# Performance work log

Measured on AMD Instinct MI355X. Metric: run time of the kernel, lower is better.

The kernel has to match this reference:

```python
import jax, jax.numpy as jnp
import numpy as np

B, C, N = 2, 6, 2048      # batch, channels (xyz+3 extra), points per cloud
K, NS = 64, 32            # top-k keypoints, ball-query group size
D = 32                    # deep feature dim (num_feat)
RADIUS = 1.0              # ball query radius (sample_and_group)
VR, VS = 1.0, 0.4         # voxelize range / step -> 6^3 = 216 candidates


def setup_inputs() -> dict:
    key = jax.random.key(0)
    ks = jax.random.split(key, 16)
    rn = lambda k, s, sc=1.0: jax.random.normal(k, s, dtype=jnp.float32) * sc
    Q, _ = jnp.linalg.qr(jax.random.normal(ks[2], (3, 3), dtype=jnp.float32))
    return {
        "src_pts": rn(ks[0], (B, C, N)),
        "tgt_pts": rn(ks[1], (B, C, N)),
        "R_init": Q,
        "t_init": rn(ks[3], (1, 3), 0.1),
        "W1": rn(ks[4], (C, 64), 0.2), "b1": jnp.zeros((64,), jnp.float32),
        "W2": rn(ks[5], (64, D), 0.2), "b2": jnp.zeros((D,), jnp.float32),
        "Wwl": rn(ks[6], (D, 1), 0.2), "bwl": jnp.zeros((1,), jnp.float32),
        "W3": rn(ks[7], (3 + D, 64), 0.2), "b3": jnp.zeros((64,), jnp.float32),
        "W4": rn(ks[8], (64, D), 0.2), "b4": jnp.zeros((D,), jnp.float32),
    }


def _fe(pts, W1, b1, W2, b2):
    # feat_extraction_layer: shared point-wise MLP. pts [B,C,N] -> xyz [B,N,3], feat [B,N,D]
    x = jnp.transpose(pts, (0, 2, 1))
    xyz = x[..., :3]
    f = jax.nn.relu(x @ W1 + b1)
    f = jax.nn.relu(f @ W2 + b2)
    return xyz, f


def _index_points(pts, idx):
    # pts [B,N,D], idx [B,K,S] -> [B,K,S,D]
    b = pts.shape[0]
    return pts[jnp.arange(b)[:, None, None], idx]


def _sqdist(a, b):
    # a [B,M,3], b [B,N,3] -> [B,M,N]
    return (jnp.sum(a * a, -1)[:, :, None] + jnp.sum(b * b, -1)[:, None, :]
            - 2.0 * jnp.einsum('bmd,bnd->bmn', a, b))


def reference(src_pts, tgt_pts, R_init, t_init, W1, b1, W2, b2, Wwl, bwl, W3, b3, W4, b4):
    b = src_pts.shape[0]
    # FE1 on source
    src_xyz, src_feat = _fe(src_pts, W1, b1, W2, b2)
    # weighting_layer: per-point saliency -> top-K keypoint indices
    w = (src_feat @ Wwl + bwl)[..., 0]                    # [B,N]
    _, kidx = jax.lax.top_k(w, K)                          # [B,K]
    src_T = jnp.transpose(src_pts, (0, 2, 1))              # [B,N,C]
    src_keypts = jnp.take_along_axis(src_T, kidx[:, :, None], axis=1)  # [B,K,C]
    centers = src_keypts[..., :3]
    # sample_and_group: ball query NS nearest-within-radius around each keypoint
    d2 = _sqdist(centers, src_xyz)                         # [B,K,N]
    negd, nn = jax.lax.top_k(-d2, NS)
    group_idx = jnp.where(-negd <= RADIUS ** 2, nn, nn[:, :, :1])
    grouped_xyz = _index_points(src_xyz, group_idx)        # [B,K,NS,3]
    keyfeats = _index_points(src_feat, group_idx)          # [B,K,NS,D]
    src_cat = jnp.concatenate([grouped_xyz - centers[:, :, None, :], keyfeats], -1)
    # FE1 on target
    tgt_xyz, tgt_feat = _fe(tgt_pts, W1, b1, W2, b2)
    # transform keypoints with initial pose, voxelize into candidate grid
    xform = jnp.einsum('ij,bkj->bki', R_init, centers) + t_init
    g = jnp.arange(int(2 * VR / VS) + 1, dtype=jnp.float32) * VS - VR   # 6 steps
    gx, gy, gz = jnp.meshgrid(g, g, g, indexing='ij')
    offs = jnp.stack([gx.ravel(), gy.ravel(), gz.ravel()], -1)          # [216,3]
    cand = xform[:, :, None, :] + offs                      # [B,K,216,3]
    nc = offs.shape[0]
    cand_flat = cand.reshape(b, K * nc, 3)
    # nearest target point per candidate -> gathered deep feature + relative offset
    d2t = _sqdist(cand_flat, tgt_xyz)                       # [B,K*216,N] (dominant buffer)
    nnt = jnp.argmin(d2t, axis=-1)                          # [B,K*216]
    nn_xyz = jnp.take_along_axis(tgt_xyz, nnt[:, :, None], axis=1)
    nn_feat = jnp.take_along_axis(tgt_feat, nnt[:, :, None], axis=1)
    rel = (nn_xyz - cand_flat).reshape(b, K, nc, 3)
    tgt_cat = jnp.concatenate([rel, nn_feat.reshape(b, K, nc, D)], -1)
    # DFE: shared MLP; src branch max-pools over the NS group
    dfe = lambda x: jax.nn.relu(jax.nn.relu(x @ W3 + b3) @ W4 + b4)
    src_dfe = jnp.max(dfe(src_cat), axis=2)                 # [B,K,D]
    tgt_dfe = dfe(tgt_cat)                                  # [B,K,216,D]
    # cpg: similarity -> softmax over candidates -> weighted centroid
    sim = jnp.einsum('bkd,bkcd->bkc', src_dfe, tgt_dfe)
    attn = jax.nn.softmax(sim, axis=-1)
    vcp = jnp.einsum('bkc,bkcd->bkd', attn, cand)           # [B,K,3]
    return src_keypts, vcp
```

## Files before the change

kernel.cpp:

```cpp
#include <hip/hip_runtime.h>
#include <math.h>

#define BB_ 2
#define CC_ 6
#define NN_ 2048
#define KK_ 64
#define NS_ 32
#define DD_ 32
#define NC_ 216
#define HH_ 64

#define OFF_SRC_PACK 0
#define OFF_TGT_PACK 16384
#define OFF_SRC_FEAT 32768
#define OFF_TGT_FEAT 163840
#define OFF_W        294912
#define OFF_CENTERS  299008
#define OFF_XFORM    299392
#define OFF_SRCDFE   299776
#define OFF_NNT      OFF_SRC_FEAT

__device__ __forceinline__ unsigned sortable_f32(float f) {
    unsigned u = __float_as_uint(f);
    return (u & 0x80000000u) ? ~u : (u | 0x80000000u);
}
__device__ __forceinline__ float unsortable_f32(unsigned s) {
    unsigned u = (s & 0x80000000u) ? (s ^ 0x80000000u) : ~s;
    return __uint_as_float(u);
}

__device__ __forceinline__ unsigned long long wave_sort64_asc(unsigned long long key, int lane) {
#pragma unroll
    for (int k = 2; k <= 64; k <<= 1) {
#pragma unroll
        for (int j = k >> 1; j > 0; j >>= 1) {
            unsigned long long other = __shfl_xor(key, j);
            bool lower = (lane & j) == 0;
            bool asc = (lane & k) == 0;
            bool takemin = (lower == asc);
            unsigned long long mn = key < other ? key : other;
            unsigned long long mx = key < other ? other : key;
            key = takemin ? mn : mx;
        }
    }
    return key;
}

__device__ __forceinline__ unsigned long long merge_keep_min64(unsigned long long a, unsigned long long b, int lane) {
    unsigned long long br = __shfl(b, 63 - lane);
    unsigned long long m = a < br ? a : br;
#pragma unroll
    for (int j = 32; j > 0; j >>= 1) {
        unsigned long long other = __shfl_xor(m, j);
        bool lower = (lane & j) == 0;
        unsigned long long mn = m < other ? m : other;
        unsigned long long mx = m < other ? other : m;
        m = lower ? mn : mx;
    }
    return m;
}

__device__ __forceinline__ void block_select64(unsigned long long kA, unsigned long long kB,
                                               unsigned long long* runs, int tid) {
    int w = tid >> 6, lane = tid & 63;
    kA = wave_sort64_asc(kA, lane);
    kB = wave_sort64_asc(kB, lane);
    unsigned long long m = merge_keep_min64(kA, kB, lane);
    runs[w * 64 + lane] = m;
    __syncthreads();
#pragma unroll
    for (int lvl = 8; lvl >= 1; lvl >>= 1) {
        unsigned long long r = 0;
        if (w < lvl) {
            unsigned long long a = runs[w * 64 + lane];
            unsigned long long b = runs[(w + lvl) * 64 + lane];
            r = merge_keep_min64(a, b, lane);
        }
        __syncthreads();
        if (w < lvl) runs[w * 64 + lane] = r;
        __syncthreads();
    }
}

__global__ void fe_kernel(const float* __restrict__ src, const float* __restrict__ tgt,
                          const float* __restrict__ W1, const float* __restrict__ b1,
                          const float* __restrict__ W2, const float* __restrict__ b2,
                          const float* __restrict__ Wwl, const float* __restrict__ bwl,
                          float* __restrict__ ws) {
    int tid = blockIdx.x * blockDim.x + threadIdx.x;
    if (tid >= 2 * BB_ * NN_) return;
    int cloud = tid / (BB_ * NN_);
    int r = tid - cloud * BB_ * NN_;
    int b = r / NN_, n = r % NN_;
    const float* pts = cloud ? tgt : src;
    float x[CC_];
#pragma unroll
    for (int c = 0; c < CC_; ++c) x[c] = pts[(b * CC_ + c) * NN_ + n];
    float bb;
    {
#pragma clang fp contract(off)
        bb = (x[0] * x[0] + x[1] * x[1]) + x[2] * x[2];
    }
    float4* pack = (float4*)(ws + (cloud ? OFF_TGT_PACK : OFF_SRC_PACK));
    pack[b * NN_ + n] = make_float4(x[0], x[1], x[2], bb);

    float h[HH_];
#pragma unroll
    for (int t = 0; t < HH_; ++t) {
        float s = b1[t];
#pragma unroll
        for (int c = 0; c < CC_; ++c) s += x[c] * W1[c * HH_ + t];
        h[t] = fmaxf(s, 0.f);
    }
    float* feat = ws + (cloud ? OFF_TGT_FEAT : OFF_SRC_FEAT) + (size_t)(b * NN_ + n) * DD_;
    float wsum = 0.f;
#pragma unroll 4
    for (int d = 0; d < DD_; ++d) {
        float s = b2[d];
#pragma unroll
        for (int t = 0; t < HH_; ++t) s += h[t] * W2[t * DD_ + d];
        s = fmaxf(s, 0.f);
        feat[d] = s;
        wsum += s * Wwl[d];
    }
    if (cloud == 0) (ws + OFF_W)[b * NN_ + n] = wsum + bwl[0];
}

__global__ void topk_kernel(const float* __restrict__ src, const float* __restrict__ R,
                            const float* __restrict__ t, float* __restrict__ ws,
                            float* __restrict__ out) {
    __shared__ unsigned long long runs[16 * 64];
    int b = blockIdx.x;
    int tid = threadIdx.x, w = tid >> 6, lane = tid & 63;
    const float* wv = ws + OFF_W + b * NN_;
    int jA = w * 128 + lane, jB = jA + 64;
    unsigned long long kA = ((unsigned long long)(~sortable_f32(wv[jA])) << 32) | (unsigned)jA;
    unsigned long long kB = ((unsigned long long)(~sortable_f32(wv[jB])) << 32) | (unsigned)jB;
    block_select64(kA, kB, runs, tid);
    if (tid < KK_) {
        int bi = (int)(runs[tid] & 0xFFFFFFFFu);
        float c3[3];
#pragma unroll
        for (int c = 0; c < CC_; ++c) {
            float v = src[(b * CC_ + c) * NN_ + bi];
            out[(b * KK_ + tid) * CC_ + c] = v;
            if (c < 3) c3[c] = v;
        }
        float* cen = ws + OFF_CENTERS + (b * KK_ + tid) * 3;
        cen[0] = c3[0]; cen[1] = c3[1]; cen[2] = c3[2];
        float* xf = ws + OFF_XFORM + (b * KK_ + tid) * 3;
#pragma unroll
        for (int i = 0; i < 3; ++i) {
#pragma clang fp contract(off)
            xf[i] = ((R[i * 3 + 0] * c3[0] + R[i * 3 + 1] * c3[1]) + R[i * 3 + 2] * c3[2]) + t[i];
        }
    }
}

__global__ void src_group_kernel(const float* __restrict__ W3, const float* __restrict__ b3,
                                 const float* __restrict__ W4, const float* __restrict__ b4,
                                 float* __restrict__ ws) {
    __shared__ unsigned long long runs[16 * 64];
    __shared__ float hs[NS_][HH_];
    __shared__ float outs[NS_][DD_];
    int bk = blockIdx.x;
    int b = bk / KK_;
    int tid = threadIdx.x, w = tid >> 6, lane = tid & 63;
    const float* cen = ws + OFF_CENTERS + bk * 3;
    float c0 = cen[0], c1 = cen[1], c2 = cen[2];
    float aa;
    {
#pragma clang fp contract(off)
        aa = (c0 * c0 + c1 * c1) + c2 * c2;
    }
    float m2x = -2.0f * c0, m2y = -2.0f * c1, m2z = -2.0f * c2;
    const float4* pack = (const float4*)(ws + OFF_SRC_PACK) + b * NN_;
    int jA = w * 128 + lane, jB = jA + 64;
    float4 pA = pack[jA], pB = pack[jB];
    float d2A, d2B;
    {
#pragma clang fp contract(off)
        d2A = (aa + pA.w) + ((m2x * pA.x + m2y * pA.y) + m2z * pA.z);
        d2B = (aa + pB.w) + ((m2x * pB.x + m2y * pB.y) + m2z * pB.z);
    }
    unsigned long long kA = ((unsigned long long)sortable_f32(d2A) << 32) | (unsigned)jA;
    unsigned long long kB = ((unsigned long long)sortable_f32(d2B) << 32) | (unsigned)jB;
    block_select64(kA, kB, runs, tid);
    const float* feats = ws + OFF_SRC_FEAT + (size_t)b * NN_ * DD_;
    unsigned long long key0 = runs[0];
#pragma unroll
    for (int ss = 0; ss < 2; ++ss) {
        int s = w * 2 + ss;
        unsigned long long key = runs[s];
        float dd = unsortable_f32((unsigned)(key >> 32));
        int j = (dd <= 1.0f) ? (int)(key & 0xFFFFFFFFu) : (int)(key0 & 0xFFFFFFFFu);
        float4 p = pack[j];
        float r0 = p.x - c0, r1 = p.y - c1, r2 = p.z - c2;
        const float* f = feats + (size_t)j * DD_;
        float acc = b3[lane] + r0 * W3[0 * HH_ + lane] + r1 * W3[1 * HH_ + lane] + r2 * W3[2 * HH_ + lane];
#pragma unroll 8
        for (int d = 0; d < DD_; ++d) acc += f[d] * W3[(3 + d) * HH_ + lane];
        hs[s][lane] = fmaxf(acc, 0.f);
    }
    __syncthreads();
    {
        int s2 = tid >> 5, di = tid & 31;
        float o = b4[di];
#pragma unroll 8
        for (int t2 = 0; t2 < HH_; ++t2) o += hs[s2][t2] * W4[t2 * DD_ + di];
        outs[s2][di] = fmaxf(o, 0.f);
    }
    __syncthreads();
    if (tid < DD_) {
        float m = -INFINITY;
#pragma unroll 8
        for (int s = 0; s < NS_; ++s) m = fmaxf(m, outs[s][tid]);
        (ws + OFF_SRCDFE)[bk * DD_ + tid] = m;
    }
}

__global__ void cand_nn_kernel(float* __restrict__ ws) {
    __shared__ float4 pk[NN_];
    int blk = blockIdx.x;
    int bk = blk >> 1;
    int half = blk & 1;
    int b = bk / KK_;
    int tid = threadIdx.x;
    const float4* pack = (const float4*)(ws + OFF_TGT_PACK) + b * NN_;
    for (int j = tid; j < NN_; j += 576) {
        pk[j ^ ((j >> 6) & 7)] = pack[j];
    }
    const float* xf = ws + OFF_XFORM + bk * 3;
    float x0 = xf[0], x1 = xf[1], x2 = xf[2];
    __syncthreads();

    int lg = tid >> 5;
    int chunk = tid & 31;
    int grp = half * 18 + lg;
    int ix = grp / 6, iy = grp % 6;
    float cx = x0 + (ix * 0.4f - 1.0f);
    float cy = x1 + (iy * 0.4f - 1.0f);
    float cxy2;
    {
#pragma clang fp contract(off)
        cxy2 = cx * cx + cy * cy;
    }
    float m2x = -2.0f * cx, m2y = -2.0f * cy;
    float aaz[6], m2z[6];
#pragma unroll
    for (int z = 0; z < 6; ++z) {
        float cz = x2 + (z * 0.4f - 1.0f);
        {
#pragma clang fp contract(off)
            aaz[z] = cxy2 + cz * cz;
        }
        m2z[z] = -2.0f * cz;
    }
    float bv[6];
    int bi[6];
#pragma unroll
    for (int z = 0; z < 6; ++z) { bv[z] = INFINITY; bi[z] = 0; }
    int base = chunk * 64;
    int sw = chunk & 7;
    for (int i = 0; i < 64; ++i) {
        int j = base + i;
        float4 p = pk[base + (i ^ sw)];
        float txy;
        {
#pragma clang fp contract(off)
            txy = m2x * p.x + m2y * p.y;
        }
#pragma unroll
        for (int z = 0; z < 6; ++z) {
            float d2;
            {
#pragma clang fp contract(off)
                d2 = (aaz[z] + p.w) + (txy + m2z[z] * p.z);
            }
            if (d2 < bv[z]) { bv[z] = d2; bi[z] = j; }
        }
    }
    int* nnt = (int*)ws + OFF_NNT + bk * NC_ + grp * 6;
#pragma unroll
    for (int z = 0; z < 6; ++z) {
        unsigned long long key = ((unsigned long long)sortable_f32(bv[z]) << 32) | (unsigned)bi[z];
#pragma unroll
        for (int m = 1; m <= 16; m <<= 1) {
            unsigned long long other = __shfl_xor(key, m);
            key = other < key ? other : key;
        }
        if (chunk == 0) nnt[z] = (int)(key & 0xFFFFFFFFu);
    }
}

__global__ void simvcp_kernel(const float* __restrict__ W3, const float* __restrict__ b3,
                              const float* __restrict__ W4, const float* __restrict__ b4,
                              float* __restrict__ ws, float* __restrict__ out) {
    __shared__ float sims[NC_];
    int bk = blockIdx.x;
    int b = bk / KK_;
    int tid = threadIdx.x;
    const float* xf = ws + OFF_XFORM + bk * 3;
    if (tid < NC_) {
        int c = tid;
        int ix = c / 36, iy = (c / 6) % 6, iz = c % 6;
        float cx = xf[0] + (ix * 0.4f - 1.0f);
        float cy = xf[1] + (iy * 0.4f - 1.0f);
        float cz = xf[2] + (iz * 0.4f - 1.0f);
        int bi = ((const int*)ws)[OFF_NNT + bk * NC_ + c];
        float4 p = ((const float4*)(ws + OFF_TGT_PACK))[b * NN_ + bi];
        float x[3 + DD_];
        x[0] = p.x - cx; x[1] = p.y - cy; x[2] = p.z - cz;
        const float* f = ws + OFF_TGT_FEAT + ((size_t)b * NN_ + bi) * DD_;
#pragma unroll
        for (int d = 0; d < DD_; ++d) x[3 + d] = f[d];
        float o[DD_];
#pragma unroll
        for (int d = 0; d < DD_; ++d) o[d] = b4[d];
        for (int t = 0; t < HH_; ++t) {
            float acc = b3[t];
#pragma unroll
            for (int cc = 0; cc < 3 + DD_; ++cc) acc += x[cc] * W3[cc * HH_ + t];
            float ht = fmaxf(acc, 0.f);
#pragma unroll
            for (int d = 0; d < DD_; ++d) o[d] += ht * W4[t * DD_ + d];
        }
        const float* sd = ws + OFF_SRCDFE + bk * DD_;
        float sim = 0.f;
#pragma unroll
        for (int d = 0; d < DD_; ++d) sim += fmaxf(o[d], 0.f) * sd[d];
        sims[c] = sim;
    }
    __syncthreads();
    if (tid < 64) {
        int lane = tid;
        float m = -INFINITY;
        for (int c = lane; c < NC_; c += 64) m = fmaxf(m, sims[c]);
#pragma unroll
        for (int sh = 32; sh; sh >>= 1) m = fmaxf(m, __shfl_xor(m, sh));
        float se = 0.f, v0 = 0.f, v1 = 0.f, v2 = 0.f;
        for (int c = lane; c < NC_; c += 64) {
            float e = expf(sims[c] - m);
            int ix = c / 36, iy = (c / 6) % 6, iz = c % 6;
            se += e;
            v0 += e * (xf[0] + (ix * 0.4f - 1.0f));
            v1 += e * (xf[1] + (iy * 0.4f - 1.0f));
            v2 += e * (xf[2] + (iz * 0.4f - 1.0f));
        }
#pragma unroll
        for (int sh = 32; sh; sh >>= 1) {
            se += __shfl_xor(se, sh);
            v0 += __shfl_xor(v0, sh);
            v1 += __shfl_xor(v1, sh);
            v2 += __shfl_xor(v2, sh);
        }
        if (lane == 0) {
            float inv = 1.0f / se;
            float* oo = out + BB_ * KK_ * CC_ + bk * 3;
            oo[0] = v0 * inv;
            oo[1] = v1 * inv;
            oo[2] = v2 * inv;
        }
    }
}

extern "C" void kernel_launch(void* const* d_in, const int* in_sizes, int n_in,
                              void* d_out, int out_size, void* d_ws, size_t ws_size,
                              hipStream_t stream) {
    const float* src = (const float*)d_in[0];
    const float* tgt = (const float*)d_in[1];
    const float* R   = (const float*)d_in[2];
    const float* t   = (const float*)d_in[3];
    const float* W1  = (const float*)d_in[4];
    const float* b1  = (const float*)d_in[5];
    const float* W2  = (const float*)d_in[6];
    const float* b2  = (const float*)d_in[7];
    const float* Wwl = (const float*)d_in[8];
    const float* bwl = (const float*)d_in[9];
    const float* W3  = (const float*)d_in[10];
    const float* b3  = (const float*)d_in[11];
    const float* W4  = (const float*)d_in[12];
    const float* b4  = (const float*)d_in[13];
    float* ws  = (float*)d_ws;
    float* out = (float*)d_out;

    fe_kernel<<<(2 * BB_ * NN_ + 127) / 128, 128, 0, stream>>>(src, tgt, W1, b1, W2, b2, Wwl, bwl, ws);
    topk_kernel<<<BB_, 1024, 0, stream>>>(src, R, t, ws, out);
    src_group_kernel<<<BB_ * KK_, 1024, 0, stream>>>(W3, b3, W4, b4, ws);
    cand_nn_kernel<<<BB_ * KK_ * 2, 576, 0, stream>>>(ws);
    simvcp_kernel<<<BB_ * KK_, 256, 0, stream>>>(W3, b3, W4, b4, ws, out);
}
```

Measured before the change: 88.92 us.

## Merge source grouping and candidate NN search into one heterogeneous kernel

Combines src_group_kernel and cand_nn_kernel into a single launch. The first 256 blocks do the candidate nearest-neighbour search and the remaining 128 blocks do ball-query grouping plus the DFE max-pool. The grouping path is reworked for 576 threads: 8 waves each sort four 64-key runs, and the merge tree is shallower. NNT output moves to its own workspace offset so it no longer aliases source features, which both branches now use concurrently. This removes one launch and lets the two independent stages overlap, at the cost of shared-memory union sizing and uneven block work.

```diff
diff --git a/kernel.cpp b/kernel.cpp
--- a/kernel.cpp
+++ b/kernel.cpp
@@ -18,7 +18,7 @@
 #define OFF_CENTERS  299008
 #define OFF_XFORM    299392
 #define OFF_SRCDFE   299776
-#define OFF_NNT      OFF_SRC_FEAT
+#define OFF_NNT      303872
 
 __device__ __forceinline__ unsigned sortable_f32(float f) {
     unsigned u = __float_as_uint(f);
@@ -60,8 +60,8 @@
     return m;
 }
 
-__device__ __forceinline__ void block_select64(unsigned long long kA, unsigned long long kB,
-                                               unsigned long long* runs, int tid) {
+__device__ __forceinline__ void block_select64_16w(unsigned long long kA, unsigned long long kB,
+                                                   unsigned long long* runs, int tid) {
     int w = tid >> 6, lane = tid & 63;
     kA = wave_sort64_asc(kA, lane);
     kB = wave_sort64_asc(kB, lane);
@@ -136,7 +136,7 @@
     int jA = w * 128 + lane, jB = jA + 64;
     unsigned long long kA = ((unsigned long long)(~sortable_f32(wv[jA])) << 32) | (unsigned)jA;
     unsigned long long kB = ((unsigned long long)(~sortable_f32(wv[jB])) << 32) | (unsigned)jB;
-    block_select64(kA, kB, runs, tid);
+    block_select64_16w(kA, kB, runs, tid);
     if (tid < KK_) {
         int bi = (int)(runs[tid] & 0xFFFFFFFFu);
         float c3[3];
@@ -157,139 +157,164 @@
     }
 }
 
-__global__ void src_group_kernel(const float* __restrict__ W3, const float* __restrict__ b3,
-                                 const float* __restrict__ W4, const float* __restrict__ b4,
-                                 float* __restrict__ ws) {
-    __shared__ unsigned long long runs[16 * 64];
-    __shared__ float hs[NS_][HH_];
-    __shared__ float outs[NS_][DD_];
-    int bk = blockIdx.x;
-    int b = bk / KK_;
-    int tid = threadIdx.x, w = tid >> 6, lane = tid & 63;
-    const float* cen = ws + OFF_CENTERS + bk * 3;
-    float c0 = cen[0], c1 = cen[1], c2 = cen[2];
-    float aa;
-    {
-#pragma clang fp contract(off)
-        aa = (c0 * c0 + c1 * c1) + c2 * c2;
-    }
-    float m2x = -2.0f * c0, m2y = -2.0f * c1, m2z = -2.0f * c2;
-    const float4* pack = (const float4*)(ws + OFF_SRC_PACK) + b * NN_;
-    int jA = w * 128 + lane, jB = jA + 64;
-    float4 pA = pack[jA], pB = pack[jB];
-    float d2A, d2B;
-    {
-#pragma clang fp contract(off)
-        d2A = (aa + pA.w) + ((m2x * pA.x + m2y * pA.y) + m2z * pA.z);
-        d2B = (aa + pB.w) + ((m2x * pB.x + m2y * pB.y) + m2z * pB.z);
-    }
-    unsigned long long kA = ((unsigned long long)sortable_f32(d2A) << 32) | (unsigned)jA;
-    unsigned long long kB = ((unsigned long long)sortable_f32(d2B) << 32) | (unsigned)jB;
-    block_select64(kA, kB, runs, tid);
-    const float* feats = ws + OFF_SRC_FEAT + (size_t)b * NN_ * DD_;
-    unsigned long long key0 = runs[0];
-#pragma unroll
-    for (int ss = 0; ss < 2; ++ss) {
-        int s = w * 2 + ss;
-        unsigned long long key = runs[s];
-        float dd = unsortable_f32((unsigned)(key >> 32));
-        int j = (dd <= 1.0f) ? (int)(key & 0xFFFFFFFFu) : (int)(key0 & 0xFFFFFFFFu);
-        float4 p = pack[j];
-        float r0 = p.x - c0, r1 = p.y - c1, r2 = p.z - c2;
-        const float* f = feats + (size_t)j * DD_;
-        float acc = b3[lane] + r0 * W3[0 * HH_ + lane] + r1 * W3[1 * HH_ + lane] + r2 * W3[2 * HH_ + lane];
+__global__ __launch_bounds__(576) void mid_kernel(const float* __restrict__ W3, const float* __restrict__ b3,
+                                                  const float* __restrict__ W4, const float* __restrict__ b4,
+                                                  float* __restrict__ ws) {
+    __shared__ union U {
+        float4 pk[NN_];
+        struct {
+            unsigned long long runs[8 * 64];
+            float hs[NS_][HH_];
+            float outs[NS_][DD_];
+        } s;
+    } u;
+    int blk = blockIdx.x;
+    int tid = threadIdx.x;
+    if (blk < 2 * BB_ * KK_) {
+        int bk = blk >> 1;
+        int half = blk & 1;
+        int b = bk / KK_;
+        const float4* pack = (const float4*)(ws + OFF_TGT_PACK) + b * NN_;
+        for (int j = tid; j < NN_; j += 576) {
+            u.pk[j ^ ((j >> 6) & 7)] = pack[j];
+        }
+        const float* xf = ws + OFF_XFORM + bk * 3;
+        float x0 = xf[0], x1 = xf[1], x2 = xf[2];
+        __syncthreads();
+
+        int lg = tid >> 5;
+        int chunk = tid & 31;
+        int grp = half * 18 + lg;
+        int ix = grp / 6, iy = grp % 6;
+        float cx = x0 + (ix * 0.4f - 1.0f);
+        float cy = x1 + (iy * 0.4f - 1.0f);
+        float cxy2;
+        {
+#pragma clang fp contract(off)
+            cxy2 = cx * cx + cy * cy;
+        }
+        float m2x = -2.0f * cx, m2y = -2.0f * cy;
+        float aaz[6], m2z[6];
+#pragma unroll
+        for (int z = 0; z < 6; ++z) {
+            float cz = x2 + (z * 0.4f - 1.0f);
+            {
+#pragma clang fp contract(off)
+                aaz[z] = cxy2 + cz * cz;
+            }
+            m2z[z] = -2.0f * cz;
+        }
+        float bv[6];
+        int bi[6];
+#pragma unroll
+        for (int z = 0; z < 6; ++z) { bv[z] = INFINITY; bi[z] = 0; }
+        int base = chunk * 64;
+        int sw = chunk & 7;
+        for (int i = 0; i < 64; ++i) {
+            int j = base + i;
+            float4 p = u.pk[base + (i ^ sw)];
+            float txy;
+            {
+#pragma clang fp contract(off)
+                txy = m2x * p.x + m2y * p.y;
+            }
+#pragma unroll
+            for (int z = 0; z < 6; ++z) {
+                float d2;
+                {
+#pragma clang fp contract(off)
+                    d2 = (aaz[z] + p.w) + (txy + m2z[z] * p.z);
+                }
+                if (d2 < bv[z]) { bv[z] = d2; bi[z] = j; }
+            }
+        }
+        int* nnt = (int*)ws + OFF_NNT + bk * NC_ + grp * 6;
+#pragma unroll
+        for (int z = 0; z < 6; ++z) {
+            unsigned long long key = ((unsigned long long)sortable_f32(bv[z]) << 32) | (unsigned)bi[z];
+#pragma unroll
+            for (int m = 1; m <= 16; m <<= 1) {
+                unsigned long long other = __shfl_xor(key, m);
+                key = other < key ? other : key;
+            }
+            if (chunk == 0) nnt[z] = (int)(key & 0xFFFFFFFFu);
+        }
+    } else {
+        int bk = blk - 2 * BB_ * KK_;
+        int b = bk / KK_;
+        int w = tid >> 6, lane = tid & 63;
+        const float* cen = ws + OFF_CENTERS + bk * 3;
+        float c0 = cen[0], c1 = cen[1], c2 = cen[2];
+        float aa;
+        {
+#pragma clang fp contract(off)
+            aa = (c0 * c0 + c1 * c1) + c2 * c2;
+        }
+        float m2x = -2.0f * c0, m2y = -2.0f * c1, m2z = -2.0f * c2;
+        const float4* pack = (const float4*)(ws + OFF_SRC_PACK) + b * NN_;
+        if (w < 8) {
+            unsigned long long k4[4];
+#pragma unroll
+            for (int q = 0; q < 4; ++q) {
+                int j = w * 256 + q * 64 + lane;
+                float4 p = pack[j];
+                float d2;
+                {
+#pragma clang fp contract(off)
+                    d2 = (aa + p.w) + ((m2x * p.x + m2y * p.y) + m2z * p.z);
+                }
+                k4[q] = ((unsigned long long)sortable_f32(d2) << 32) | (unsigned)j;
+            }
+            unsigned long long m1 = merge_keep_min64(wave_sort64_asc(k4[0], lane),
+                                                     wave_sort64_asc(k4[1], lane), lane);
+            unsigned long long m2 = merge_keep_min64(wave_sort64_asc(k4[2], lane),
+                                                     wave_sort64_asc(k4[3], lane), lane);
+            u.s.runs[w * 64 + lane] = merge_keep_min64(m1, m2, lane);
+        }
+        __syncthreads();
+#pragma unroll
+        for (int lvl = 4; lvl >= 1; lvl >>= 1) {
+            unsigned long long r = 0;
+            if (w < lvl) {
+                r = merge_keep_min64(u.s.runs[w * 64 + lane], u.s.runs[(w + lvl) * 64 + lane], lane);
+            }
+            __syncthreads();
+            if (w < lvl) u.s.runs[w * 64 + lane] = r;
+            __syncthreads();
+        }
+        const float* feats = ws + OFF_SRC_FEAT + (size_t)b * NN_ * DD_;
+        unsigned long long key0 = u.s.runs[0];
+        if (w < 8) {
+#pragma unroll
+            for (int ss = 0; ss < 4; ++ss) {
+                int s = w * 4 + ss;
+                unsigned long long key = u.s.runs[s];
+                float dd = unsortable_f32((unsigned)(key >> 32));
+                int j = (dd <= 1.0f) ? (int)(key & 0xFFFFFFFFu) : (int)(key0 & 0xFFFFFFFFu);
+                float4 p = pack[j];
+                float r0 = p.x - c0, r1 = p.y - c1, r2 = p.z - c2;
+                const float* f = feats + (size_t)j * DD_;
+                float acc = b3[lane] + r0 * W3[0 * HH_ + lane] + r1 * W3[1 * HH_ + lane] + r2 * W3[2 * HH_ + lane];
 #pragma unroll 8
-        for (int d = 0; d < DD_; ++d) acc += f[d] * W3[(3 + d) * HH_ + lane];
-        hs[s][lane] = fmaxf(acc, 0.f);
-    }
-    __syncthreads();
-    {
-        int s2 = tid >> 5, di = tid & 31;
-        float o = b4[di];
+                for (int d = 0; d < DD_; ++d) acc += f[d] * W3[(3 + d) * HH_ + lane];
+                u.s.hs[s][lane] = fmaxf(acc, 0.f);
+            }
+        }
+        __syncthreads();
+        for (int idx = tid; idx < NS_ * DD_; idx += 576) {
+            int s2 = idx >> 5, di = idx & 31;
+            float o = b4[di];
 #pragma unroll 8
-        for (int t2 = 0; t2 < HH_; ++t2) o += hs[s2][t2] * W4[t2 * DD_ + di];
-        outs[s2][di] = fmaxf(o, 0.f);
-    }
-    __syncthreads();
-    if (tid < DD_) {
-        float m = -INFINITY;
+            for (int t2 = 0; t2 < HH_; ++t2) o += u.s.hs[s2][t2] * W4[t2 * DD_ + di];
+            u.s.outs[s2][di] = fmaxf(o, 0.f);
+        }
+        __syncthreads();
+        if (tid < DD_) {
+            float m = -INFINITY;
 #pragma unroll 8
-        for (int s = 0; s < NS_; ++s) m = fmaxf(m, outs[s][tid]);
-        (ws + OFF_SRCDFE)[bk * DD_ + tid] = m;
-    }
-}
-
-__global__ void cand_nn_kernel(float* __restrict__ ws) {
-    __shared__ float4 pk[NN_];
-    int blk = blockIdx.x;
-    int bk = blk >> 1;
-    int half = blk & 1;
-    int b = bk / KK_;
-    int tid = threadIdx.x;
-    const float4* pack = (const float4*)(ws + OFF_TGT_PACK) + b * NN_;
-    for (int j = tid; j < NN_; j += 576) {
-        pk[j ^ ((j >> 6) & 7)] = pack[j];
-    }
-    const float* xf = ws + OFF_XFORM + bk * 3;
-    float x0 = xf[0], x1 = xf[1], x2 = xf[2];
-    __syncthreads();
-
-    int lg = tid >> 5;
-    int chunk = tid & 31;
-    int grp = half * 18 + lg;
-    int ix = grp / 6, iy = grp % 6;
-    float cx = x0 + (ix * 0.4f - 1.0f);
-    float cy = x1 + (iy * 0.4f - 1.0f);
-    float cxy2;
-    {
-#pragma clang fp contract(off)
-        cxy2 = cx * cx + cy * cy;
-    }
-    float m2x = -2.0f * cx, m2y = -2.0f * cy;
-    float aaz[6], m2z[6];
-#pragma unroll
-    for (int z = 0; z < 6; ++z) {
-        float cz = x2 + (z * 0.4f - 1.0f);
-        {
-#pragma clang fp contract(off)
-            aaz[z] = cxy2 + cz * cz;
-        }
-        m2z[z] = -2.0f * cz;
-    }
-    float bv[6];
-    int bi[6];
-#pragma unroll
-    for (int z = 0; z < 6; ++z) { bv[z] = INFINITY; bi[z] = 0; }
-    int base = chunk * 64;
-    int sw = chunk & 7;
-    for (int i = 0; i < 64; ++i) {
-        int j = base + i;
-        float4 p = pk[base + (i ^ sw)];
-        float txy;
-        {
-#pragma clang fp contract(off)
-            txy = m2x * p.x + m2y * p.y;
-        }
-#pragma unroll
-        for (int z = 0; z < 6; ++z) {
-            float d2;
-            {
-#pragma clang fp contract(off)
-                d2 = (aaz[z] + p.w) + (txy + m2z[z] * p.z);
-            }
-            if (d2 < bv[z]) { bv[z] = d2; bi[z] = j; }
-        }
-    }
-    int* nnt = (int*)ws + OFF_NNT + bk * NC_ + grp * 6;
-#pragma unroll
-    for (int z = 0; z < 6; ++z) {
-        unsigned long long key = ((unsigned long long)sortable_f32(bv[z]) << 32) | (unsigned)bi[z];
-#pragma unroll
-        for (int m = 1; m <= 16; m <<= 1) {
-            unsigned long long other = __shfl_xor(key, m);
-            key = other < key ? other : key;
-        }
-        if (chunk == 0) nnt[z] = (int)(key & 0xFFFFFFFFu);
+            for (int s = 0; s < NS_; ++s) m = fmaxf(m, u.s.outs[s][tid]);
+            (ws + OFF_SRCDFE)[bk * DD_ + tid] = m;
+        }
     }
 }
 
@@ -386,7 +411,6 @@
 
     fe_kernel<<<(2 * BB_ * NN_ + 127) / 128, 128, 0, stream>>>(src, tgt, W1, b1, W2, b2, Wwl, bwl, ws);
     topk_kernel<<<BB_, 1024, 0, stream>>>(src, R, t, ws, out);
-    src_group_kernel<<<BB_ * KK_, 1024, 0, stream>>>(W3, b3, W4, b4, ws);
-    cand_nn_kernel<<<BB_ * KK_ * 2, 576, 0, stream>>>(ws);
+    mid_kernel<<<2 * BB_ * KK_ + BB_ * KK_, 576, 0, stream>>>(W3, b3, W4, b4, ws);
     simvcp_kernel<<<BB_ * KK_, 256, 0, stream>>>(W3, b3, W4, b4, ws, out);
 }
```

Result: faster. 82.53 us (-7.2%).
